# Kernel tuning notes

Measured on AMD Instinct MI355X. Metric: run time of the kernel, lower is better.

The kernel has to match this reference:

```python
import jax, jax.numpy as jnp
import numpy as np

HEADS = 8
DIM_HEAD = 64
DIM = 512
HIDDEN = HEADS * DIM_HEAD  # 512
SCALE = DIM_HEAD ** -0.5
EPS = 1e-12  # F.normalize clamp


def setup_inputs() -> dict:
    key = jax.random.key(0)
    ks = jax.random.split(key, 7)
    b, c, n = 8, DIM, 4096
    x = jax.random.normal(ks[0], (b, c, n), dtype=jnp.float32)
    # 1x1 Conv1d weights are [out_ch, in_ch] matmuls over channel dim
    Wq = jax.random.normal(ks[1], (HIDDEN, DIM), dtype=jnp.float32) * (DIM ** -0.5)
    Wk = jax.random.normal(ks[2], (HIDDEN, DIM), dtype=jnp.float32) * (DIM ** -0.5)
    Wv = jax.random.normal(ks[3], (HIDDEN, DIM), dtype=jnp.float32) * (DIM ** -0.5)
    Wout = jax.random.normal(ks[4], (DIM, HIDDEN), dtype=jnp.float32) * (HIDDEN ** -0.5)
    bout = jax.random.normal(ks[5], (DIM,), dtype=jnp.float32) * 0.01
    g = jnp.ones((DIM,), dtype=jnp.float32)  # RMSNorm gain, torch init = ones
    return {"x": x, "Wq": Wq, "Wk": Wk, "Wv": Wv, "Wout": Wout, "bout": bout, "g": g}


def reference(x, Wq, Wk, Wv, Wout, bout, g):
    b, c, n = x.shape
    # 1x1 conv projections: [b, hidden, n]
    q = jnp.einsum('oc,bcn->bon', Wq, x)
    k = jnp.einsum('oc,bcn->bon', Wk, x)
    v = jnp.einsum('oc,bcn->bon', Wv, x)
    # split heads: b (h d) n -> b h d n
    q = q.reshape(b, HEADS, DIM_HEAD, n)
    k = k.reshape(b, HEADS, DIM_HEAD, n)
    v = v.reshape(b, HEADS, DIM_HEAD, n)
    # dual softmax linear attention
    q = jax.nn.softmax(q, axis=-2) * SCALE      # softmax over feature dim d
    k = jax.nn.softmax(k, axis=-1)              # softmax over sequence dim n
    ctx = jnp.einsum('bhdn,bhen->bhde', k, v)   # per-head [d, e] context
    out = jnp.einsum('bhde,bhdn->bhen', ctx, q) # [b, h, e, n]
    out = out.reshape(b, HIDDEN, n)
    # output 1x1 conv with bias
    out = jnp.einsum('oc,bcn->bon', Wout, out) + bout[None, :, None]
    # RMSNorm: F.normalize(x, dim=1) * g * sqrt(c)
    norm = jnp.sqrt(jnp.sum(out * out, axis=1, keepdims=True))
    out = out / jnp.maximum(norm, EPS)
    out = out * g[None, :, None] * jnp.sqrt(jnp.asarray(c, out.dtype))
    return out
```

## Files before the change

### kernel.cpp

```cpp
#include <hip/hip_runtime.h>
#include <math.h>

#define NB 8
#define CDIM 512
#define NSEQ 4096
#define NHEAD 8
#define DHEAD 64
#define SCALE_Q 0.125f
#define SQRT_C  22.627416997969522f

typedef unsigned short u16;
typedef short bf16x8 __attribute__((ext_vector_type(8)));
typedef float f32x4 __attribute__((ext_vector_type(4)));

__device__ __forceinline__ u16 f2bf(float f) {
    unsigned u = __float_as_uint(f);
    u = u + 0x7FFFu + ((u >> 16) & 1u);
    return (u16)(u >> 16);
}
__device__ __forceinline__ float bf2f(u16 h) {
    return __uint_as_float(((unsigned)h) << 16);
}
__device__ __forceinline__ void split_bf(float v, u16& h, u16& l) {
    h = f2bf(v);
    l = f2bf(v - bf2f(h));
}

__device__ __forceinline__ void gload_lds16(const void* g, void* l) {
    __builtin_amdgcn_global_load_lds(
        (const __attribute__((address_space(1))) void*)g,
        (__attribute__((address_space(3))) void*)l, 16, 0, 0);
}

template<bool BIAS>
__global__ __launch_bounds__(256)
void gemm_split(const u16* __restrict__ Ahi, const u16* __restrict__ Alo,
                const u16* __restrict__ Bhi, const u16* __restrict__ Blo,
                float* __restrict__ C, const float* __restrict__ bias,
                int N, int K,
                long long sA, long long sB, long long sC)
{
    Ahi += (long long)blockIdx.z * sA; Alo += (long long)blockIdx.z * sA;
    Bhi += (long long)blockIdx.z * sB; Blo += (long long)blockIdx.z * sB;
    C   += (long long)blockIdx.z * sC;

    __shared__ __align__(16) char sb[32768];

    const int tid = threadIdx.x;
    const int w = tid >> 6, lane = tid & 63;
    const int wr = w >> 1, wc = w & 1;
    const int row0 = blockIdx.y * 128, col0 = blockIdx.x * 128;

    const int rsub = lane >> 3;
    const int jsel = (lane & 7) ^ rsub;
    const int koff = (jsel & 3) << 3;
    const u16* aops = (jsel < 4) ? Ahi : Alo;
    const u16* bops = (jsel < 4) ? Bhi : Blo;

    const int r = lane & 15, h = lane >> 4;
    const int s_hi = (h ^ (r & 7)) << 4;
    const int s_lo = ((h + 4) ^ (r & 7)) << 4;
    int offA[4][2], offB[4][2];
#pragma unroll
    for (int i = 0; i < 4; ++i) {
        const int ra = (wr * 64 + i * 16 + r) * 128;
        offA[i][0] = ra + s_hi;  offA[i][1] = ra + s_lo;
        const int rb = 16384 + (wc * 64 + i * 16 + r) * 128;
        offB[i][0] = rb + s_hi;  offB[i][1] = rb + s_lo;
    }

    f32x4 acc[4][4];
#pragma unroll
    for (int i = 0; i < 4; ++i)
#pragma unroll
        for (int j = 0; j < 4; ++j) acc[i][j] = (f32x4){0.f, 0.f, 0.f, 0.f};

    for (int k0 = 0; k0 < K; k0 += 32) {
        __syncthreads();
#pragma unroll
        for (int i = 0; i < 4; ++i) {
            const int t = 4 * w + i;
            gload_lds16(aops + (long long)(row0 + 8 * t + rsub) * K + k0 + koff,
                        sb + t * 1024);
            gload_lds16(bops + (long long)(col0 + 8 * t + rsub) * K + k0 + koff,
                        sb + 16384 + t * 1024);
        }
        __syncthreads();

        bf16x8 ah[4], al[4], bh[4], bl[4];
#pragma unroll
        for (int i = 0; i < 4; ++i) {
            ah[i] = *(const bf16x8*)(sb + offA[i][0]);
            al[i] = *(const bf16x8*)(sb + offA[i][1]);
            bh[i] = *(const bf16x8*)(sb + offB[i][0]);
            bl[i] = *(const bf16x8*)(sb + offB[i][1]);
        }
#pragma unroll
        for (int mi = 0; mi < 4; ++mi)
#pragma unroll
            for (int ni = 0; ni < 4; ++ni) {
                acc[mi][ni] = __builtin_amdgcn_mfma_f32_16x16x32_bf16(ah[mi], bh[ni], acc[mi][ni], 0, 0, 0);
                acc[mi][ni] = __builtin_amdgcn_mfma_f32_16x16x32_bf16(ah[mi], bl[ni], acc[mi][ni], 0, 0, 0);
                acc[mi][ni] = __builtin_amdgcn_mfma_f32_16x16x32_bf16(al[mi], bh[ni], acc[mi][ni], 0, 0, 0);
            }
    }

#pragma unroll
    for (int mi = 0; mi < 4; ++mi) {
        const int rowm = row0 + wr * 64 + mi * 16 + h * 4;
#pragma unroll
        for (int ni = 0; ni < 4; ++ni) {
            const int coln = col0 + wc * 64 + ni * 16 + r;
#pragma unroll
            for (int reg = 0; reg < 4; ++reg) {
                float v = acc[mi][ni][reg];
                if (BIAS) v += bias[rowm + reg];
                C[(long long)(rowm + reg) * N + coln] = v;
            }
        }
    }
}

__global__ __launch_bounds__(256)
void cvt_split(const float* __restrict__ in, u16* __restrict__ hi,
               u16* __restrict__ lo, int n)
{
    for (int i = blockIdx.x * 256 + threadIdx.x; i < n; i += 65536) {
        u16 h, l; split_bf(in[i], h, l);
        hi[i] = h; lo[i] = l;
    }
}

__global__ __launch_bounds__(256)
void xpose_split(const float* __restrict__ x, u16* __restrict__ thi,
                 u16* __restrict__ tlo)
{
    __shared__ float t[64][65];
    const int tid = threadIdx.x;
    const int b = blockIdx.z, c0 = blockIdx.y * 64, n0 = blockIdx.x * 64;
    const float* xb = x + ((long long)b * CDIM + c0) * NSEQ + n0;
#pragma unroll
    for (int i = 0; i < 16; ++i) {
        const int f = tid + i * 256;
        t[f >> 6][f & 63] = xb[(long long)(f >> 6) * NSEQ + (f & 63)];
    }
    __syncthreads();
#pragma unroll
    for (int i = 0; i < 8; ++i) {
        const int f = tid + i * 256;
        const int nl = f >> 5, c2 = (f & 31) << 1;
        u16 h0, l0, h1, l1;
        split_bf(t[c2][nl], h0, l0);
        split_bf(t[c2 + 1][nl], h1, l1);
        const long long o = ((long long)b * NSEQ + n0 + nl) * CDIM + c0 + c2;
        ushort2 hv; hv.x = h0; hv.y = h1; *(ushort2*)&thi[o] = hv;
        ushort2 lv; lv.x = l0; lv.y = l1; *(ushort2*)&tlo[o] = lv;
    }
}

__global__ __launch_bounds__(256)
void kstats_kernel(const float* __restrict__ k,
                   float* __restrict__ kmax, float* __restrict__ kinv)
{
    const long long row = blockIdx.x;
    const float* kr = k + row * (long long)NSEQ;
    const int tid = threadIdx.x;
    const int lane = tid & 63, wv = tid >> 6;

    float4 v[4];
    float m = -INFINITY;
#pragma unroll
    for (int i = 0; i < 4; ++i) {
        v[i] = ((const float4*)kr)[tid + i * 256];
        m = fmaxf(m, fmaxf(fmaxf(v[i].x, v[i].y), fmaxf(v[i].z, v[i].w)));
    }
#pragma unroll
    for (int off = 32; off; off >>= 1) m = fmaxf(m, __shfl_xor(m, off));

    __shared__ float red[8];
    if (lane == 0) red[wv] = m;
    __syncthreads();
    m = fmaxf(fmaxf(red[0], red[1]), fmaxf(red[2], red[3]));

    float s = 0.f;
#pragma unroll
    for (int i = 0; i < 4; ++i)
        s += __expf(v[i].x - m) + __expf(v[i].y - m)
           + __expf(v[i].z - m) + __expf(v[i].w - m);
#pragma unroll
    for (int off = 32; off; off >>= 1) s += __shfl_xor(s, off);
    if (lane == 0) red[4 + wv] = s;
    __syncthreads();
    if (tid == 0) {
        kmax[row] = m;
        kinv[row] = 1.0f / (red[4] + red[5] + red[6] + red[7]);
    }
}

__global__ __launch_bounds__(256)
void qsoftmax_t(const float* __restrict__ q, u16* __restrict__ phi,
                u16* __restrict__ plo)
{
    __shared__ float t[64][65];
    __shared__ float red[8][64];
    const int tid = threadIdx.x;
    const int n0 = blockIdx.x * 64, hh = blockIdx.y, b = blockIdx.z;
    const float* qb = q + ((long long)b * CDIM + hh * DHEAD) * NSEQ + n0;
#pragma unroll
    for (int i = 0; i < 16; ++i) {
        const int f = tid + i * 256;
        t[f >> 6][f & 63] = qb[(long long)(f >> 6) * NSEQ + (f & 63)];
    }
    __syncthreads();
    const int nl = tid & 63, part = tid >> 6;
    float m = -INFINITY;
#pragma unroll
    for (int dd = 0; dd < 16; ++dd) m = fmaxf(m, t[part * 16 + dd][nl]);
    red[part][nl] = m;
    __syncthreads();
    m = fmaxf(fmaxf(red[0][nl], red[1][nl]), fmaxf(red[2][nl], red[3][nl]));
    float s = 0.f;
#pragma unroll
    for (int dd = 0; dd < 16; ++dd) {
        const float e = __expf(t[part * 16 + dd][nl] - m);
        t[part * 16 + dd][nl] = e;
        s += e;
    }
    red[4 + part][nl] = s;
    __syncthreads();
#pragma unroll
    for (int i = 0; i < 8; ++i) {
        const int f = tid + i * 256;
        const int n2 = f >> 5, c2 = (f & 31) << 1;
        const float inv = SCALE_Q / (red[4][n2] + red[5][n2] + red[6][n2] + red[7][n2]);
        u16 h0, l0, h1, l1;
        split_bf(t[c2][n2] * inv, h0, l0);
        split_bf(t[c2 + 1][n2] * inv, h1, l1);
        const long long o = ((long long)b * NSEQ + n0 + n2) * CDIM + hh * DHEAD + c2;
        ushort2 hv; hv.x = h0; hv.y = h1; *(ushort2*)&phi[o] = hv;
        ushort2 lv; lv.x = l0; lv.y = l1; *(ushort2*)&plo[o] = lv;
    }
}

__global__ __launch_bounds__(256)
void ctx_part_kernel(const float* __restrict__ k, const float* __restrict__ v,
                     const float* __restrict__ kmax, const float* __restrict__ kinv,
                     float* __restrict__ ctx_part)
{
    const int chunk = blockIdx.x;
    const int bh = blockIdx.y;
    const int b = bh >> 3, h = bh & 7;

    __shared__ float kt[64 * 64];
    __shared__ float vt[64 * 64];

    const int tid = threadIdx.x;
    const int td = tid & 15, te = tid >> 4;
    const long long rowbase = (long long)b * CDIM + h * DHEAD;

    float acc[4][4];
#pragma unroll
    for (int i = 0; i < 4; ++i)
#pragma unroll
        for (int j = 0; j < 4; ++j) acc[i][j] = 0.f;

    for (int tile = 0; tile < 8; ++tile) {
        const int n0 = chunk * 512 + tile * 64;
        __syncthreads();
#pragma unroll
        for (int i = 0; i < 4; ++i) {
            const int f = tid + i * 256;
            const int row = f >> 4;
            const int c4 = (f & 15) << 2;
            const int cs = c4 ^ (((row >> 2) & 7) << 2);
            float4 kv = *(const float4*)&k[(rowbase + row) * (long long)NSEQ + n0 + c4];
            const float m_ = kmax[rowbase + row];
            const float s_ = kinv[rowbase + row];
            kv.x = __expf(kv.x - m_) * s_; kv.y = __expf(kv.y - m_) * s_;
            kv.z = __expf(kv.z - m_) * s_; kv.w = __expf(kv.w - m_) * s_;
            *(float4*)&kt[row * 64 + cs] = kv;
            *(float4*)&vt[row * 64 + cs] =
                *(const float4*)&v[(rowbase + row) * (long long)NSEQ + n0 + c4];
        }
        __syncthreads();

#pragma unroll
        for (int nn = 0; nn < 64; nn += 4) {
            float4 ka[4], vb[4];
#pragma unroll
            for (int i = 0; i < 4; ++i) {
                const int d = td * 4 + i;
                ka[i] = *(const float4*)&kt[d * 64 + (nn ^ (((d >> 2) & 7) << 2))];
            }
#pragma unroll
            for (int j = 0; j < 4; ++j) {
                const int e = te * 4 + j;
                vb[j] = *(const float4*)&vt[e * 64 + (nn ^ (((e >> 2) & 7) << 2))];
            }
#pragma unroll
            for (int i = 0; i < 4; ++i)
#pragma unroll
                for (int j = 0; j < 4; ++j) {
                    acc[i][j] = fmaf(ka[i].x, vb[j].x, acc[i][j]);
                    acc[i][j] = fmaf(ka[i].y, vb[j].y, acc[i][j]);
                    acc[i][j] = fmaf(ka[i].z, vb[j].z, acc[i][j]);
                    acc[i][j] = fmaf(ka[i].w, vb[j].w, acc[i][j]);
                }
        }
    }

    float* cbase = ctx_part + (long long)chunk * 262144 + ((long long)bh << 12);
#pragma unroll
    for (int i = 0; i < 4; ++i)
#pragma unroll
        for (int j = 0; j < 4; ++j)
            cbase[(td * 4 + i) * 64 + te * 4 + j] = acc[i][j];
}

__global__ __launch_bounds__(256)
void ctx_reduce(const float* __restrict__ part, float* __restrict__ ctx)
{
    const int i = blockIdx.x * 256 + threadIdx.x;
    float s = 0.f;
#pragma unroll
    for (int c = 0; c < 8; ++c) s += part[(long long)c * 262144 + i];
    ctx[i] = s;
}

__global__ __launch_bounds__(256)
void w2_split(const float* __restrict__ Wout, const float* __restrict__ ctx,
              u16* __restrict__ w2hi, u16* __restrict__ w2lo)
{
    const int o0 = blockIdx.x * 128;
    const int h = blockIdx.y, b = blockIdx.z;
    const int tid = threadIdx.x;

    __shared__ float ctxT[64 * 65];
    __shared__ float WoutS[128 * 65];

    const float* csrc = ctx + (((long long)b * NHEAD + h) << 12);
#pragma unroll
    for (int i = 0; i < 16; ++i) {
        const int f = tid + i * 256;
        ctxT[(f & 63) * 65 + (f >> 6)] = csrc[f];
    }
#pragma unroll
    for (int i = 0; i < 32; ++i) {
        const int f = tid + i * 256;
        WoutS[(f >> 6) * 65 + (f & 63)] =
            Wout[(long long)(o0 + (f >> 6)) * CDIM + h * DHEAD + (f & 63)];
    }
    __syncthreads();

    const int d = tid & 63, og = tid >> 6;
    float acc[32];
#pragma unroll
    for (int oo = 0; oo < 32; ++oo) acc[oo] = 0.f;

    for (int e = 0; e < 64; ++e) {
        const float c = ctxT[e * 65 + d];
#pragma unroll
        for (int oo = 0; oo < 32; ++oo)
            acc[oo] = fmaf(WoutS[(og * 32 + oo) * 65 + e], c, acc[oo]);
    }
#pragma unroll
    for (int oo = 0; oo < 32; ++oo) {
        const int o = o0 + og * 32 + oo;
        u16 hh, ll; split_bf(acc[oo], hh, ll);
        const long long idx = ((long long)b * CDIM + o) * CDIM + h * DHEAD + d;
        w2hi[idx] = hh; w2lo[idx] = ll;
    }
}

__global__ __launch_bounds__(256)
void rmsnorm_kernel(const float* __restrict__ pre, const float* __restrict__ g,
                    float* __restrict__ out)
{
    const int tid = threadIdx.x;
    const int b = blockIdx.y;
    const int n = blockIdx.x * 64 + (tid & 63);
    const int cg = tid >> 6;
    const float* pb = pre + (long long)b * CDIM * NSEQ + n;
    float* ob = out + (long long)b * CDIM * NSEQ + n;

    float ss = 0.f;
    for (int c = cg * 128; c < cg * 128 + 128; ++c) {
        const float x = pb[(long long)c * NSEQ];
        ss = fmaf(x, x, ss);
    }
    __shared__ float red[4][64];
    red[cg][tid & 63] = ss;
    __syncthreads();
    const float tot = red[0][tid & 63] + red[1][tid & 63]
                    + red[2][tid & 63] + red[3][tid & 63];
    const float rn = SQRT_C / fmaxf(sqrtf(tot), 1e-12f);

    for (int c = cg * 128; c < cg * 128 + 128; ++c)
        ob[(long long)c * NSEQ] = pb[(long long)c * NSEQ] * rn * g[c];
}

extern "C" void kernel_launch(void* const* d_in, const int* in_sizes, int n_in,
                              void* d_out, int out_size, void* d_ws, size_t ws_size,
                              hipStream_t stream)
{
    const float* x    = (const float*)d_in[0];
    const float* Wq   = (const float*)d_in[1];
    const float* Wk   = (const float*)d_in[2];
    const float* Wv   = (const float*)d_in[3];
    const float* Wout = (const float*)d_in[4];
    const float* bout = (const float*)d_in[5];
    const float* g    = (const float*)d_in[6];
    float* out = (float*)d_out;

    const long long PB = (long long)CDIM * NSEQ;
    const long long QK = (long long)NB * PB;

    const long long C_FLOATS = 8192 + 9LL * 262144 + 11LL * 262144;
    const size_t WS_NEEDED = (size_t)(2 * QK + C_FLOATS) * sizeof(float);
    if (ws_size < WS_NEEDED) return;

    float* ws = (float*)d_ws;
    u16* xthi = (u16*)ws;
    u16* xtlo = xthi + QK;
    float* buf1 = ws + QK;
    float* kmax = ws + 2 * QK;
    float* kinv = kmax + 4096;
    float* ctx  = kinv + 4096;
    float* ctxp = ctx + 262144;
    u16* whi    = (u16*)(ctxp + 8 * 262144);
    u16* wlo    = whi + 3 * 262144;
    u16* w2hi   = wlo + 3 * 262144;
    u16* w2lo   = w2hi + (long long)NB * 262144;

    float* kbuf = buf1;
    float* vbuf = out;
    float* qbuf = buf1;
    float* outpre = buf1;
    u16* phi = xthi;
    u16* plo = xtlo;

    cvt_split<<<256, 256, 0, stream>>>(Wq, whi,              wlo,              262144);
    cvt_split<<<256, 256, 0, stream>>>(Wk, whi + 262144,     wlo + 262144,     262144);
    cvt_split<<<256, 256, 0, stream>>>(Wv, whi + 2 * 262144, wlo + 2 * 262144, 262144);
    xpose_split<<<dim3(64, 8, 8), 256, 0, stream>>>(x, xthi, xtlo);

    const dim3 gg(NSEQ / 128, CDIM / 128, NB);

    gemm_split<false><<<gg, 256, 0, stream>>>(whi + 262144, wlo + 262144,
                                              xthi, xtlo, kbuf, nullptr,
                                              NSEQ, CDIM, 0, PB, PB);
    kstats_kernel<<<dim3(NB * CDIM), 256, 0, stream>>>(kbuf, kmax, kinv);

    gemm_split<false><<<gg, 256, 0, stream>>>(whi + 2 * 262144, wlo + 2 * 262144,
                                              xthi, xtlo, vbuf, nullptr,
                                              NSEQ, CDIM, 0, PB, PB);
    ctx_part_kernel<<<dim3(8, NB * NHEAD), 256, 0, stream>>>(kbuf, vbuf, kmax, kinv, ctxp);
    ctx_reduce<<<1024, 256, 0, stream>>>(ctxp, ctx);

    gemm_split<false><<<gg, 256, 0, stream>>>(whi, wlo,
                                              xthi, xtlo, qbuf, nullptr,
                                              NSEQ, CDIM, 0, PB, PB);
    qsoftmax_t<<<dim3(NSEQ / 64, NHEAD, NB), 256, 0, stream>>>(qbuf, phi, plo);

    w2_split<<<dim3(4, NHEAD, NB), 256, 0, stream>>>(Wout, ctx, w2hi, w2lo);
    gemm_split<true><<<gg, 256, 0, stream>>>(w2hi, w2lo, phi, plo, outpre, bout,
                                             NSEQ, CDIM, 262144, PB, PB);

    rmsnorm_kernel<<<dim3(NSEQ / 64, NB), 256, 0, stream>>>(outpre, g, out);
}
```

Baseline: 491.2 us.

## Fuse softmax statistics and RMSNorm sum-of-squares into GEMM epilogues

Adds templated GEMM epilogues. The K projection now emits per-tile partial max/sum, which a small kernel combines. The Q projection applies the feature-dim softmax in registers and writes the bf16 hi/lo split directly. The output projection adds the bias and emits partial sums of squares. These replace the separate kstats, qsoftmax and rmsnorm reduction passes, which each re-read large fp32 buffers, and the three weight conversions are merged into one launch. The price is extra register pressure and shuffles in the GEMM epilogue, plus a rmsnorm launch of only 32 blocks that serially walks 512 channels, which may limit parallelism.

```diff
diff --git a/kernel.cpp b/kernel.cpp
--- a/kernel.cpp
+++ b/kernel.cpp
@@ -32,11 +32,13 @@
         (__attribute__((address_space(3))) void*)l, 16, 0, 0);
 }
 
-template<bool BIAS>
+template<int EPI>
 __global__ __launch_bounds__(256)
 void gemm_split(const u16* __restrict__ Ahi, const u16* __restrict__ Alo,
                 const u16* __restrict__ Bhi, const u16* __restrict__ Blo,
                 float* __restrict__ C, const float* __restrict__ bias,
+                u16* __restrict__ P0, u16* __restrict__ P1,
+                float* __restrict__ S0, float* __restrict__ S1,
                 int N, int K,
                 long long sA, long long sB, long long sC)
 {
@@ -105,6 +107,63 @@
             }
     }
 
+    const int bx = blockIdx.x, by = blockIdx.y, bz = blockIdx.z;
+
+    if constexpr (EPI == 2) {
+#pragma unroll
+        for (int ni = 0; ni < 4; ++ni) {
+            float cm = -INFINITY;
+#pragma unroll
+            for (int mi = 0; mi < 4; ++mi)
+#pragma unroll
+                for (int reg = 0; reg < 4; ++reg)
+                    cm = fmaxf(cm, acc[mi][ni][reg]);
+            cm = fmaxf(cm, __shfl_xor(cm, 16));
+            cm = fmaxf(cm, __shfl_xor(cm, 32));
+            float cs = 0.f;
+#pragma unroll
+            for (int mi = 0; mi < 4; ++mi)
+#pragma unroll
+                for (int reg = 0; reg < 4; ++reg) {
+                    const float e = __expf(acc[mi][ni][reg] - cm);
+                    acc[mi][ni][reg] = e;
+                    cs += e;
+                }
+            cs += __shfl_xor(cs, 16);
+            cs += __shfl_xor(cs, 32);
+            const float inv = SCALE_Q / cs;
+            const long long coln = col0 + wc * 64 + ni * 16 + r;
+            const long long obase = ((long long)bz * NSEQ + coln) * CDIM
+                                    + row0 + wr * 64 + h * 4;
+#pragma unroll
+            for (int mi = 0; mi < 4; ++mi) {
+                u16 hv0, lv0, hv1, lv1, hv2, lv2, hv3, lv3;
+                split_bf(acc[mi][ni][0] * inv, hv0, lv0);
+                split_bf(acc[mi][ni][1] * inv, hv1, lv1);
+                split_bf(acc[mi][ni][2] * inv, hv2, lv2);
+                split_bf(acc[mi][ni][3] * inv, hv3, lv3);
+                ushort4 hq; hq.x = hv0; hq.y = hv1; hq.z = hv2; hq.w = hv3;
+                ushort4 lq; lq.x = lv0; lq.y = lv1; lq.z = lv2; lq.w = lv3;
+                *(ushort4*)&P0[obase + mi * 16] = hq;
+                *(ushort4*)&P1[obase + mi * 16] = lq;
+            }
+        }
+        return;
+    }
+
+    if constexpr (EPI == 3) {
+#pragma unroll
+        for (int mi = 0; mi < 4; ++mi) {
+            const int rowm = row0 + wr * 64 + mi * 16 + h * 4;
+#pragma unroll
+            for (int reg = 0; reg < 4; ++reg) {
+                const float bv = bias[rowm + reg];
+#pragma unroll
+                for (int ni = 0; ni < 4; ++ni) acc[mi][ni][reg] += bv;
+            }
+        }
+    }
+
 #pragma unroll
     for (int mi = 0; mi < 4; ++mi) {
         const int rowm = row0 + wr * 64 + mi * 16 + h * 4;
@@ -112,22 +171,85 @@
         for (int ni = 0; ni < 4; ++ni) {
             const int coln = col0 + wc * 64 + ni * 16 + r;
 #pragma unroll
+            for (int reg = 0; reg < 4; ++reg)
+                C[(long long)(rowm + reg) * N + coln] = acc[mi][ni][reg];
+        }
+    }
+
+    if constexpr (EPI == 1) {
+#pragma unroll
+        for (int mi = 0; mi < 4; ++mi)
+#pragma unroll
             for (int reg = 0; reg < 4; ++reg) {
-                float v = acc[mi][ni][reg];
-                if (BIAS) v += bias[rowm + reg];
-                C[(long long)(rowm + reg) * N + coln] = v;
-            }
-        }
-    }
-}
-
-__global__ __launch_bounds__(256)
-void cvt_split(const float* __restrict__ in, u16* __restrict__ hi,
-               u16* __restrict__ lo, int n)
-{
-    for (int i = blockIdx.x * 256 + threadIdx.x; i < n; i += 65536) {
-        u16 h, l; split_bf(in[i], h, l);
-        hi[i] = h; lo[i] = l;
+                float m = -INFINITY;
+#pragma unroll
+                for (int ni = 0; ni < 4; ++ni) m = fmaxf(m, acc[mi][ni][reg]);
+                m = fmaxf(m, __shfl_xor(m, 1));
+                m = fmaxf(m, __shfl_xor(m, 2));
+                m = fmaxf(m, __shfl_xor(m, 4));
+                m = fmaxf(m, __shfl_xor(m, 8));
+                float s = 0.f;
+#pragma unroll
+                for (int ni = 0; ni < 4; ++ni) s += __expf(acc[mi][ni][reg] - m);
+                s += __shfl_xor(s, 1);
+                s += __shfl_xor(s, 2);
+                s += __shfl_xor(s, 4);
+                s += __shfl_xor(s, 8);
+                if (r == 0) {
+                    const int srow = bz * CDIM + row0 + wr * 64 + mi * 16 + h * 4 + reg;
+                    S0[srow * 64 + bx * 2 + wc] = m;
+                    S1[srow * 64 + bx * 2 + wc] = s;
+                }
+            }
+    }
+
+    if constexpr (EPI == 3) {
+#pragma unroll
+        for (int ni = 0; ni < 4; ++ni) {
+            float ss = 0.f;
+#pragma unroll
+            for (int mi = 0; mi < 4; ++mi)
+#pragma unroll
+                for (int reg = 0; reg < 4; ++reg)
+                    ss += acc[mi][ni][reg] * acc[mi][ni][reg];
+            ss += __shfl_xor(ss, 16);
+            ss += __shfl_xor(ss, 32);
+            if (h == 0) {
+                const int coln = col0 + wc * 64 + ni * 16 + r;
+                S0[(long long)(by * 2 + wr) * (NB * NSEQ)
+                   + (long long)bz * NSEQ + coln] = ss;
+            }
+        }
+    }
+}
+
+__global__ __launch_bounds__(256)
+void kfin_kernel(const float* __restrict__ pmax, const float* __restrict__ psum,
+                 float* __restrict__ kmax, float* __restrict__ kinv)
+{
+    const int row = blockIdx.x * 256 + threadIdx.x;
+    float m = -INFINITY;
+#pragma unroll
+    for (int i = 0; i < 64; ++i) m = fmaxf(m, pmax[row * 64 + i]);
+    float s = 0.f;
+#pragma unroll
+    for (int i = 0; i < 64; ++i)
+        s += psum[row * 64 + i] * __expf(pmax[row * 64 + i] - m);
+    kmax[row] = m;
+    kinv[row] = 1.0f / s;
+}
+
+__global__ __launch_bounds__(256)
+void cvt3(const float* __restrict__ Wq, const float* __restrict__ Wk,
+          const float* __restrict__ Wv, u16* __restrict__ hi,
+          u16* __restrict__ lo)
+{
+    const float* src = (blockIdx.y == 0) ? Wq : ((blockIdx.y == 1) ? Wk : Wv);
+    u16* hd = hi + (long long)blockIdx.y * 262144;
+    u16* ld = lo + (long long)blockIdx.y * 262144;
+    for (int i = blockIdx.x * 256 + threadIdx.x; i < 262144; i += 16384) {
+        u16 h, l; split_bf(src[i], h, l);
+        hd[i] = h; ld[i] = l;
     }
 }
 
@@ -155,90 +277,6 @@
         const long long o = ((long long)b * NSEQ + n0 + nl) * CDIM + c0 + c2;
         ushort2 hv; hv.x = h0; hv.y = h1; *(ushort2*)&thi[o] = hv;
         ushort2 lv; lv.x = l0; lv.y = l1; *(ushort2*)&tlo[o] = lv;
-    }
-}
-
-__global__ __launch_bounds__(256)
-void kstats_kernel(const float* __restrict__ k,
-                   float* __restrict__ kmax, float* __restrict__ kinv)
-{
-    const long long row = blockIdx.x;
-    const float* kr = k + row * (long long)NSEQ;
-    const int tid = threadIdx.x;
-    const int lane = tid & 63, wv = tid >> 6;
-
-    float4 v[4];
-    float m = -INFINITY;
-#pragma unroll
-    for (int i = 0; i < 4; ++i) {
-        v[i] = ((const float4*)kr)[tid + i * 256];
-        m = fmaxf(m, fmaxf(fmaxf(v[i].x, v[i].y), fmaxf(v[i].z, v[i].w)));
-    }
-#pragma unroll
-    for (int off = 32; off; off >>= 1) m = fmaxf(m, __shfl_xor(m, off));
-
-    __shared__ float red[8];
-    if (lane == 0) red[wv] = m;
-    __syncthreads();
-    m = fmaxf(fmaxf(red[0], red[1]), fmaxf(red[2], red[3]));
-
-    float s = 0.f;
-#pragma unroll
-    for (int i = 0; i < 4; ++i)
-        s += __expf(v[i].x - m) + __expf(v[i].y - m)
-           + __expf(v[i].z - m) + __expf(v[i].w - m);
-#pragma unroll
-    for (int off = 32; off; off >>= 1) s += __shfl_xor(s, off);
-    if (lane == 0) red[4 + wv] = s;
-    __syncthreads();
-    if (tid == 0) {
-        kmax[row] = m;
-        kinv[row] = 1.0f / (red[4] + red[5] + red[6] + red[7]);
-    }
-}
-
-__global__ __launch_bounds__(256)
-void qsoftmax_t(const float* __restrict__ q, u16* __restrict__ phi,
-                u16* __restrict__ plo)
-{
-    __shared__ float t[64][65];
-    __shared__ float red[8][64];
-    const int tid = threadIdx.x;
-    const int n0 = blockIdx.x * 64, hh = blockIdx.y, b = blockIdx.z;
-    const float* qb = q + ((long long)b * CDIM + hh * DHEAD) * NSEQ + n0;
-#pragma unroll
-    for (int i = 0; i < 16; ++i) {
-        const int f = tid + i * 256;
-        t[f >> 6][f & 63] = qb[(long long)(f >> 6) * NSEQ + (f & 63)];
-    }
-    __syncthreads();
-    const int nl = tid & 63, part = tid >> 6;
-    float m = -INFINITY;
-#pragma unroll
-    for (int dd = 0; dd < 16; ++dd) m = fmaxf(m, t[part * 16 + dd][nl]);
-    red[part][nl] = m;
-    __syncthreads();
-    m = fmaxf(fmaxf(red[0][nl], red[1][nl]), fmaxf(red[2][nl], red[3][nl]));
-    float s = 0.f;
-#pragma unroll
-    for (int dd = 0; dd < 16; ++dd) {
-        const float e = __expf(t[part * 16 + dd][nl] - m);
-        t[part * 16 + dd][nl] = e;
-        s += e;
-    }
-    red[4 + part][nl] = s;
-    __syncthreads();
-#pragma unroll
-    for (int i = 0; i < 8; ++i) {
-        const int f = tid + i * 256;
-        const int n2 = f >> 5, c2 = (f & 31) << 1;
-        const float inv = SCALE_Q / (red[4][n2] + red[5][n2] + red[6][n2] + red[7][n2]);
-        u16 h0, l0, h1, l1;
-        split_bf(t[c2][n2] * inv, h0, l0);
-        split_bf(t[c2 + 1][n2] * inv, h1, l1);
-        const long long o = ((long long)b * NSEQ + n0 + n2) * CDIM + hh * DHEAD + c2;
-        ushort2 hv; hv.x = h0; hv.y = h1; *(ushort2*)&phi[o] = hv;
-        ushort2 lv; lv.x = l0; lv.y = l1; *(ushort2*)&plo[o] = lv;
     }
 }
 
@@ -373,30 +411,31 @@
 }
 
 __global__ __launch_bounds__(256)
-void rmsnorm_kernel(const float* __restrict__ pre, const float* __restrict__ g,
-                    float* __restrict__ out)
-{
-    const int tid = threadIdx.x;
+void rmsnorm2(const float* __restrict__ pre, const float* __restrict__ ssp,
+              const float* __restrict__ g, float* __restrict__ out)
+{
     const int b = blockIdx.y;
-    const int n = blockIdx.x * 64 + (tid & 63);
-    const int cg = tid >> 6;
-    const float* pb = pre + (long long)b * CDIM * NSEQ + n;
-    float* ob = out + (long long)b * CDIM * NSEQ + n;
-
-    float ss = 0.f;
-    for (int c = cg * 128; c < cg * 128 + 128; ++c) {
-        const float x = pb[(long long)c * NSEQ];
-        ss = fmaf(x, x, ss);
-    }
-    __shared__ float red[4][64];
-    red[cg][tid & 63] = ss;
-    __syncthreads();
-    const float tot = red[0][tid & 63] + red[1][tid & 63]
-                    + red[2][tid & 63] + red[3][tid & 63];
-    const float rn = SQRT_C / fmaxf(sqrtf(tot), 1e-12f);
-
-    for (int c = cg * 128; c < cg * 128 + 128; ++c)
-        ob[(long long)c * NSEQ] = pb[(long long)c * NSEQ] * rn * g[c];
+    const int n4 = (blockIdx.x * 256 + threadIdx.x) * 4;
+    float4 ss = {0.f, 0.f, 0.f, 0.f};
+#pragma unroll
+    for (int p = 0; p < 8; ++p) {
+        const float4 v = *(const float4*)&ssp[((long long)p * NB + b) * NSEQ + n4];
+        ss.x += v.x; ss.y += v.y; ss.z += v.z; ss.w += v.w;
+    }
+    float4 rn;
+    rn.x = SQRT_C / fmaxf(sqrtf(ss.x), 1e-12f);
+    rn.y = SQRT_C / fmaxf(sqrtf(ss.y), 1e-12f);
+    rn.z = SQRT_C / fmaxf(sqrtf(ss.z), 1e-12f);
+    rn.w = SQRT_C / fmaxf(sqrtf(ss.w), 1e-12f);
+
+    const long long base = (long long)b * CDIM * NSEQ + n4;
+    for (int c = 0; c < CDIM; ++c) {
+        float4 v = *(const float4*)&pre[base + (long long)c * NSEQ];
+        const float gc = g[c];
+        v.x *= rn.x * gc; v.y *= rn.y * gc;
+        v.z *= rn.z * gc; v.w *= rn.w * gc;
+        *(float4*)&out[base + (long long)c * NSEQ] = v;
+    }
 }
 
 extern "C" void kernel_launch(void* const* d_in, const int* in_sizes, int n_in,
@@ -432,39 +471,43 @@
     u16* w2hi   = wlo + 3 * 262144;
     u16* w2lo   = w2hi + (long long)NB * 262144;
 
+    float* pmax = ctxp;
+    float* psum = ctxp + 262144;
+    float* ssp  = ctxp;
+
     float* kbuf = buf1;
+    float* outpre = buf1;
     float* vbuf = out;
-    float* qbuf = buf1;
-    float* outpre = buf1;
-    u16* phi = xthi;
-    u16* plo = xtlo;
-
-    cvt_split<<<256, 256, 0, stream>>>(Wq, whi,              wlo,              262144);
-    cvt_split<<<256, 256, 0, stream>>>(Wk, whi + 262144,     wlo + 262144,     262144);
-    cvt_split<<<256, 256, 0, stream>>>(Wv, whi + 2 * 262144, wlo + 2 * 262144, 262144);
+    u16* phi = (u16*)out;
+    u16* plo = phi + QK;
+
+    cvt3<<<dim3(64, 3), 256, 0, stream>>>(Wq, Wk, Wv, whi, wlo);
     xpose_split<<<dim3(64, 8, 8), 256, 0, stream>>>(x, xthi, xtlo);
 
     const dim3 gg(NSEQ / 128, CDIM / 128, NB);
 
-    gemm_split<false><<<gg, 256, 0, stream>>>(whi + 262144, wlo + 262144,
-                                              xthi, xtlo, kbuf, nullptr,
-                                              NSEQ, CDIM, 0, PB, PB);
-    kstats_kernel<<<dim3(NB * CDIM), 256, 0, stream>>>(kbuf, kmax, kinv);
-
-    gemm_split<false><<<gg, 256, 0, stream>>>(whi + 2 * 262144, wlo + 2 * 262144,
-                                              xthi, xtlo, vbuf, nullptr,
-                                              NSEQ, CDIM, 0, PB, PB);
+    gemm_split<1><<<gg, 256, 0, stream>>>(whi + 262144, wlo + 262144,
+                                          xthi, xtlo, kbuf, nullptr,
+                                          nullptr, nullptr, pmax, psum,
+                                          NSEQ, CDIM, 0, PB, PB);
+    kfin_kernel<<<dim3(16), 256, 0, stream>>>(pmax, psum, kmax, kinv);
+
+    gemm_split<0><<<gg, 256, 0, stream>>>(whi + 2 * 262144, wlo + 2 * 262144,
+                                          xthi, xtlo, vbuf, nullptr,
+                                          nullptr, nullptr, nullptr, nullptr,
+                                          NSEQ, CDIM, 0, PB, PB);
     ctx_part_kernel<<<dim3(8, NB * NHEAD), 256, 0, stream>>>(kbuf, vbuf, kmax, kinv, ctxp);
     ctx_reduce<<<1024, 256, 0, stream>>>(ctxp, ctx);
 
-    gemm_split<false><<<gg, 256, 0, stream>>>(whi, wlo,
-                                              xthi, xtlo, qbuf, nullptr,
-                                              NSEQ, CDIM, 0, PB, PB);
-    qsoftmax_t<<<dim3(NSEQ / 64, NHEAD, NB), 256, 0, stream>>>(qbuf, phi, plo);
+    gemm_split<2><<<gg, 256, 0, stream>>>(whi, wlo,
+                                          xthi, xtlo, buf1, nullptr,
+                                          phi, plo, nullptr, nullptr,
+                                          NSEQ, CDIM, 0, PB, PB);
 
     w2_split<<<dim3(4, NHEAD, NB), 256, 0, stream>>>(Wout, ctx, w2hi, w2lo);
-    gemm_split<true><<<gg, 256, 0, stream>>>(w2hi, w2lo, phi, plo, outpre, bout,
-                                             NSEQ, CDIM, 262144, PB, PB);
-
-    rmsnorm_kernel<<<dim3(NSEQ / 64, NB), 256, 0, stream>>>(outpre, g, out);
-}
+    gemm_split<3><<<gg, 256, 0, stream>>>(w2hi, w2lo, phi, plo, outpre, bout,
+                                          nullptr, nullptr, ssp, nullptr,
+                                          NSEQ, CDIM, 262144, PB, PB);
+
+    rmsnorm2<<<dim3(4, NB), 256, 0, stream>>>(outpre, ssp, g, out);
+}
```

New measurement: 598.1 us. 21.8% more time.
